# Kernel tuning notes

Measured on AMD Instinct MI355X. Metric: run time of the kernel, lower is better.

## Reference

```python
import jax, jax.numpy as jnp
import numpy as np

DIM = 1024
HEADS = 8
DIM_HEAD = 128
SCALE = DIM_HEAD ** -0.5
EPS = 1e-10
ROPE_THETA = 10000.0


def _rope_cos_sin(n, d, dtype):
    # lucidrains rotary-embedding-torch: interleaved freqs, repeated pairwise
    inv_freq = 1.0 / (ROPE_THETA ** (jnp.arange(0, d, 2, dtype=jnp.float32) / d))
    freqs = jnp.arange(n, dtype=jnp.float32)[:, None] * inv_freq[None, :]  # [n, d/2]
    freqs = jnp.repeat(freqs, 2, axis=-1)  # [n, d] interleaved (f0,f0,f1,f1,...)
    return jnp.cos(freqs).astype(dtype), jnp.sin(freqs).astype(dtype)


def _rotate_half(x):
    x = x.reshape(*x.shape[:-1], -1, 2)
    x1, x2 = x[..., 0], x[..., 1]
    return jnp.stack((-x2, x1), axis=-1).reshape(*x.shape[:-2], -1)


def _apply_rope(t, cos, sin):
    return t * cos + _rotate_half(t) * sin


def setup_inputs() -> dict:
    key = jax.random.key(0)
    k1, k2, k3, k4, k5 = jax.random.split(key, 5)
    b, n = 2, 2048
    return {
        "x": jax.random.normal(k1, (b, n, DIM), dtype=jnp.float32),
        "gamma": jnp.ones((DIM,), dtype=jnp.float32),
        "w_qkv": jax.random.normal(k2, (3 * HEADS * DIM_HEAD, DIM), dtype=jnp.float32) * 0.02,
        "w_out": jax.random.normal(k3, (DIM, HEADS * DIM_HEAD), dtype=jnp.float32) * 0.02,
        "head_gates": jnp.ones((HEADS,), dtype=jnp.float32) * 10.0,
        "mem_kv": jax.random.normal(k4, (b, HEADS, DIM_HEAD, DIM_HEAD), dtype=jnp.float32),
        "mem_norm": jax.random.uniform(k5, (b, HEADS, DIM_HEAD), dtype=jnp.float32) + 0.5,
    }


def _retrieve(t, mem_kv, mem_norm):
    # t: [b,h,n,dk] -> [b,h,n,dv]
    numer = jnp.einsum('bhnk,bhkv->bhnv', t, mem_kv)
    denom = jnp.einsum('bhnk,bhk->bhn', t, mem_norm)
    return numer / jnp.clip(denom, EPS, None)[..., None]


def reference(x, gamma, w_qkv, w_out, head_gates, mem_kv, mem_norm):
    b, n, _ = x.shape
    # RMSNorm (F.normalize * sqrt(dim) * gamma)
    xn = x / jnp.clip(jnp.linalg.norm(x, axis=-1, keepdims=True), 1e-12, None)
    xn = xn * (DIM ** 0.5) * gamma
    # qkv projection, split heads: 'b n (qkv h d) -> qkv b h n d'
    qkv = xn @ w_qkv.T  # [b,n,3*h*d]
    qkv = qkv.reshape(b, n, 3, HEADS, DIM_HEAD).transpose(2, 0, 3, 1, 4)
    q, k, v = qkv[0], qkv[1], qkv[2]

    cos, sin = _rope_cos_sin(n, DIM_HEAD, x.dtype)
    q_rot = _apply_rope(q * SCALE, cos, sin)
    k_rot = _apply_rope(k, cos, sin)

    sim = jnp.einsum('bhid,bhjd->bhij', q_rot, k_rot)
    causal = jnp.triu(jnp.ones((n, n), dtype=bool), 1)
    sim = jnp.where(causal, jnp.finfo(sim.dtype).min, sim)
    attn = jax.nn.softmax(sim, axis=-1)
    out = jnp.einsum('bhij,bhjd->bhid', attn, v)

    # linear-attention feature map on UNrotated, unscaled q/k
    qf = jax.nn.elu(q) + 1.0
    kf = jax.nn.elu(k) + 1.0

    # gated retrieval from past memories
    mem_out = _retrieve(qf, mem_kv, mem_norm)
    gates = jax.nn.sigmoid(head_gates)[None, :, None, None]
    out = out * gates + mem_out * (1.0 - gates)

    out = out.transpose(0, 2, 1, 3).reshape(b, n, HEADS * DIM_HEAD)
    out = out @ w_out.T

    # delta rule memory update
    delta_v = _retrieve(kf, mem_kv, mem_norm)
    v_new = v - delta_v
    new_kv = jnp.einsum('bhnk,bhnv->bhkv', kf, v_new) + mem_kv
    new_norm = kf.sum(axis=2) + mem_norm
    return out, new_kv, new_norm
```

## Files before the change

kernel.cpp:

```cpp
#include <hip/hip_runtime.h>
#include <hip/hip_bf16.h>

#define B_ 2
#define N_ 2048
#define H_ 8
#define DH_ 128
#define D_ 1024
#define NO_ 3072
#define SCALE_ 0.08838834764831845f

typedef __bf16 bf16;
typedef __bf16 bf16x4 __attribute__((ext_vector_type(4)));
typedef __bf16 bf16x8 __attribute__((ext_vector_type(8)));
typedef float f32x4 __attribute__((ext_vector_type(4)));

__device__ inline f32x4 mfma16(bf16x8 a, bf16x8 b, f32x4 c) {
  return __builtin_amdgcn_mfma_f32_16x16x32_bf16(a, b, c, 0, 0, 0);
}

__device__ inline float elu1(float x) { return x > 0.f ? x + 1.f : __expf(x); }

__device__ inline void gl_lds16(const bf16* g, bf16* l) {
  __builtin_amdgcn_global_load_lds(
      (const __attribute__((address_space(1))) unsigned int*)g,
      (__attribute__((address_space(3))) unsigned int*)l, 16, 0, 0);
}

__global__ __launch_bounds__(256) void k_rmsnorm(const float* __restrict__ x,
                                                 const float* __restrict__ gamma,
                                                 bf16* __restrict__ xn) {
  int row = blockIdx.x;
  int t = threadIdx.x;
  const float4* xr = (const float4*)(x + (size_t)row * D_);
  float4 xv = xr[t];
  float ss = xv.x*xv.x + xv.y*xv.y + xv.z*xv.z + xv.w*xv.w;
#pragma unroll
  for (int m = 1; m < 64; m <<= 1) ss += __shfl_xor(ss, m);
  __shared__ float sred[4];
  if ((t & 63) == 0) sred[t >> 6] = ss;
  __syncthreads();
  float tot = sred[0] + sred[1] + sred[2] + sred[3];
  float scale = 32.0f / fmaxf(sqrtf(tot), 1e-12f);
  float4 gv = ((const float4*)gamma)[t];
  bf16x4 ov;
  ov[0] = (bf16)(xv.x * scale * gv.x);
  ov[1] = (bf16)(xv.y * scale * gv.y);
  ov[2] = (bf16)(xv.z * scale * gv.z);
  ov[3] = (bf16)(xv.w * scale * gv.w);
  *(bf16x4*)(xn + (size_t)row * D_ + t * 4) = ov;
}

__global__ void k_cvtW(const float4* __restrict__ a, bf16x4* __restrict__ oa, int na4,
                       const float4* __restrict__ b, bf16x4* __restrict__ ob, int nb4) {
  int i = blockIdx.x * blockDim.x + threadIdx.x;
  if (i < na4) {
    float4 v = a[i];
    bf16x4 o;
    o[0] = (bf16)v.x; o[1] = (bf16)v.y; o[2] = (bf16)v.z; o[3] = (bf16)v.w;
    oa[i] = o;
  } else {
    int j = i - na4;
    if (j < nb4) {
      float4 v = b[j];
      bf16x4 o;
      o[0] = (bf16)v.x; o[1] = (bf16)v.y; o[2] = (bf16)v.z; o[3] = (bf16)v.w;
      ob[j] = o;
    }
  }
}

__global__ __launch_bounds__(256) void k_mkvT(const float* __restrict__ mem_kv,
                                              const float* __restrict__ mem_norm,
                                              bf16* __restrict__ mkvT,
                                              float* __restrict__ out_kv,
                                              float* __restrict__ out_norm) {
  int bh = blockIdx.x;
  int t = threadIdx.x;
  int v = t & 127, khalf = t >> 7;
  const float* src = mem_kv + (size_t)bh * DH_ * DH_;
  bf16* dst = mkvT + (size_t)bh * DH_ * DH_ + (size_t)v * DH_ + khalf * 64;
#pragma unroll
  for (int kk8 = 0; kk8 < 8; kk8++) {
    int k0 = khalf * 64 + kk8 * 8;
    bf16x8 o;
#pragma unroll
    for (int e = 0; e < 8; e++) o[e] = (bf16)src[(size_t)(k0 + e) * DH_ + v];
    *(bf16x8*)(dst + kk8 * 8) = o;
  }
  const float4* s4 = (const float4*)src;
  float4* d4 = (float4*)(out_kv + (size_t)bh * DH_ * DH_);
#pragma unroll
  for (int i = 0; i < 16; i++) d4[t + i * 256] = s4[t + i * 256];
  if (t < DH_) out_norm[(size_t)bh * DH_ + t] = mem_norm[(size_t)bh * DH_ + t];
}

template <typename OT>
__global__ __launch_bounds__(256) void k_gemm_lds(const bf16* __restrict__ A,
                                                  const bf16* __restrict__ B,
                                                  OT* __restrict__ C,
                                                  int M, int Nn, int K) {
  __shared__ __align__(16) bf16 sA[128 * 32];
  __shared__ __align__(16) bf16 sB[128 * 32];
  int t = threadIdx.x;
  int w = t >> 6, lane = t & 63, quad = lane >> 4, l16 = lane & 15;
  int lin = blockIdx.y * gridDim.x + blockIdx.x;
  int cpx = (gridDim.x * gridDim.y) >> 3;
  int swz = (lin & 7) * cpx + (lin >> 3);
  int bx = swz % gridDim.x, by = swz / gridDim.x;
  int m0 = by * 128, n0 = bx * 128;
  int wr = (w & 1) * 64, wc = (w >> 1) * 64;
  f32x4 zf = {0.f, 0.f, 0.f, 0.f};
  f32x4 acc[4][4];
#pragma unroll
  for (int a = 0; a < 4; a++)
#pragma unroll
    for (int c = 0; c < 4; c++) acc[a][c] = zf;
  int srow = w * 16 + (lane >> 2);
  int scol = (lane & 3) * 8;
  const bf16* gA = A + (size_t)(m0 + srow) * K + scol;
  const bf16* gB = B + (size_t)(n0 + srow) * K + scol;
  bf16* lA0 = sA + (size_t)w * 16 * 32;
  bf16* lA1 = sA + (size_t)(64 + w * 16) * 32;
  bf16* lB0 = sB + (size_t)w * 16 * 32;
  bf16* lB1 = sB + (size_t)(64 + w * 16) * 32;
  for (int k0 = 0; k0 < K; k0 += 32) {
    __syncthreads();
    gl_lds16(gA + k0, lA0);
    gl_lds16(gA + (size_t)64 * K + k0, lA1);
    gl_lds16(gB + k0, lB0);
    gl_lds16(gB + (size_t)64 * K + k0, lB1);
    __syncthreads();
    bf16x8 af[4], bfr[4];
#pragma unroll
    for (int mt = 0; mt < 4; mt++)
      af[mt] = *(const bf16x8*)(sA + (wr + mt * 16 + l16) * 32 + quad * 8);
#pragma unroll
    for (int nt = 0; nt < 4; nt++)
      bfr[nt] = *(const bf16x8*)(sB + (wc + nt * 16 + l16) * 32 + quad * 8);
#pragma unroll
    for (int mt = 0; mt < 4; mt++)
#pragma unroll
      for (int nt = 0; nt < 4; nt++)
        acc[mt][nt] = mfma16(af[mt], bfr[nt], acc[mt][nt]);
  }
#pragma unroll
  for (int mt = 0; mt < 4; mt++)
#pragma unroll
    for (int nt = 0; nt < 4; nt++) {
      int row = m0 + wr + mt * 16 + quad * 4;
      int col = n0 + wc + nt * 16 + l16;
      OT* cp = C + (size_t)row * Nn + col;
#pragma unroll
      for (int r = 0; r < 4; r++) cp[(size_t)r * Nn] = (OT)acc[mt][nt][r];
    }
}

__global__ __launch_bounds__(256) void k_prep2(const bf16* __restrict__ qkv,
                                               const float* __restrict__ mem_norm,
                                               bf16* __restrict__ qr, bf16* __restrict__ kr,
                                               bf16* __restrict__ vT, bf16* __restrict__ kfT,
                                               float* __restrict__ qden, float* __restrict__ kden) {
  __shared__ __align__(16) bf16 sQ[64 * 136], sK[64 * 136], sV[64 * 136];
  __shared__ float smn[128];
  int n0 = blockIdx.x * 64, h = blockIdx.y, b = blockIdx.z;
  size_t bh = (size_t)b * H_ + h;
  int t = threadIdx.x;
#pragma unroll
  for (int p = 0; p < 4; p++) {
    int i = p * 256 + t;
    int row = i >> 4, c16 = i & 15;
    size_t base = ((size_t)b * N_ + n0 + row) * NO_ + (size_t)h * DH_;
    ((uint4*)sQ)[row * 17 + c16] = *((const uint4*)(qkv + base) + c16);
    ((uint4*)sK)[row * 17 + c16] = *((const uint4*)(qkv + base + D_) + c16);
    ((uint4*)sV)[row * 17 + c16] = *((const uint4*)(qkv + base + 2 * D_) + c16);
  }
  if (t < 128) smn[t] = mem_norm[bh * DH_ + t];
  __syncthreads();
  int row = t >> 1, h2 = t & 1, d0 = h2 * 64;
  int n = n0 + row;
  float sq = 0.f, sk = 0.f;
  const float cexp = 13.287712379549449f / 128.0f;
#pragma unroll 2
  for (int c = 0; c < 8; c++) {
    bf16x8 q8 = *(const bf16x8*)(sQ + row * 136 + d0 + c * 8);
    bf16x8 k8 = *(const bf16x8*)(sK + row * 136 + d0 + c * 8);
    bf16x8 qo, ko, kf8;
#pragma unroll
    for (int e = 0; e < 8; e += 2) {
      int d = d0 + c * 8 + e;
      float invf = exp2f(-(float)d * cexp);
      float ang = (float)n * invf;
      float sn, cs;
      __sincosf(ang, &sn, &cs);
      float qx = (float)q8[e] * SCALE_, qy = (float)q8[e + 1] * SCALE_;
      qo[e]     = (bf16)(qx * cs - qy * sn);
      qo[e + 1] = (bf16)(qy * cs + qx * sn);
      float kx = (float)k8[e], ky = (float)k8[e + 1];
      ko[e]     = (bf16)(kx * cs - ky * sn);
      ko[e + 1] = (bf16)(ky * cs + kx * sn);
      float f0 = elu1(kx), f1 = elu1(ky);
      kf8[e] = (bf16)f0; kf8[e + 1] = (bf16)f1;
      sk += f0 * smn[d] + f1 * smn[d + 1];
      sq += elu1((float)q8[e]) * smn[d] + elu1((float)q8[e + 1]) * smn[d + 1];
    }
    *(bf16x8*)(qr + (bh * N_ + n) * DH_ + d0 + c * 8) = qo;
    *(bf16x8*)(kr + (bh * N_ + n) * DH_ + d0 + c * 8) = ko;
    *(bf16x8*)(sK + row * 136 + d0 + c * 8) = kf8;
  }
  sq += __shfl_xor(sq, 1);
  sk += __shfl_xor(sk, 1);
  if (h2 == 0) { qden[bh * N_ + n] = sq; kden[bh * N_ + n] = sk; }
  __syncthreads();
  int d = t >> 1, part = t & 1;
#pragma unroll
  for (int v8 = 0; v8 < 4; v8++) {
    bf16x8 okf, ov;
#pragma unroll
    for (int e = 0; e < 8; e++) {
      int nn = part * 32 + v8 * 8 + e;
      okf[e] = sK[nn * 136 + d];
      ov[e]  = sV[nn * 136 + d];
    }
    size_t o = (bh * DH_ + d) * N_ + n0 + part * 32 + v8 * 8;
    *(bf16x8*)(kfT + o) = okf;
    *(bf16x8*)(vT + o)  = ov;
  }
}

__global__ __launch_bounds__(256) void k_attn2(const bf16* __restrict__ qr,
                                               const bf16* __restrict__ kr,
                                               const bf16* __restrict__ vT,
                                               bf16* __restrict__ attn_out,
                                               bf16* __restrict__ pO,
                                               float* __restrict__ pstat) {
  __shared__ __align__(16) bf16 sK[64 * 128];
  __shared__ __align__(16) bf16 sV[128 * 64];
  int L = blockIdx.x;
  int x = (L & 7) * 160 + (L >> 3);
  size_t bh = x / 80;
  int e = x % 80;
  int qt, c;
  if (e < 32)      { qt = 31 - (e >> 2); c = e & 3; }
  else if (e < 56) { int u = e - 32; qt = 23 - u / 3; c = u % 3; }
  else if (e < 72) { int u = e - 56; qt = 15 - (u >> 1); c = u & 1; }
  else             { qt = 7 - (e - 72); c = 0; }
  int jt0 = c * 8;
  int jt1 = min(jt0 + 8, qt + 1);

  int t = threadIdx.x;
  int w = t >> 6, lane = t & 63, quad = lane >> 4, l16 = lane & 15;
  int qlo = qt * 64 + w * 16;

  bf16x8 qfrag[4];
  const bf16* qrow = qr + (bh * N_ + qlo + l16) * DH_;
#pragma unroll
  for (int s = 0; s < 4; s++) qfrag[s] = *(const bf16x8*)(qrow + s * 32 + quad * 8);

  f32x4 zf = {0.f, 0.f, 0.f, 0.f};
  f32x4 o[8];
#pragma unroll
  for (int i = 0; i < 8; i++) o[i] = zf;
  float mrow = -1e30f, lrow = 0.f;

  int krow = lane >> 4, kc16 = lane & 15;
  int vrow = lane >> 3, vc8 = lane & 7;

  for (int jt = jt0; jt < jt1; jt++) {
    __syncthreads();
#pragma unroll
    for (int j = 0; j < 4; j++) {
      int prow = w * 16 + j * 4 + krow;
      int grow = (prow & 32) | ((prow & 12) << 1) | ((prow & 16) >> 2) | (prow & 3);
      const bf16* src = kr + (bh * N_ + (size_t)jt * 64 + grow) * DH_ + (kc16 ^ (prow & 7)) * 8;
      gl_lds16(src, sK + (w * 16 + j * 4) * 128);
    }
#pragma unroll
    for (int j = 0; j < 4; j++) {
      int row = w * 32 + j * 8 + vrow;
      const bf16* src = vT + (bh * DH_ + row) * N_ + (size_t)jt * 64 + (vc8 ^ (row & 7)) * 8;
      gl_lds16(src, sV + (w * 32 + j * 8) * 64);
    }
    __syncthreads();

    f32x4 sf[4];
#pragma unroll
    for (int nt = 0; nt < 4; nt++) sf[nt] = zf;
    __builtin_amdgcn_s_setprio(1);
#pragma unroll
    for (int s = 0; s < 4; s++) {
#pragma unroll
      for (int nt = 0; nt < 4; nt++) {
        int row = nt * 16 + l16;
        bf16x8 kf = *(const bf16x8*)(sK + row * 128 + ((s * 32 + quad * 8) ^ ((row & 7) << 3)));
        sf[nt] = mfma16(kf, qfrag[s], sf[nt]);
      }
    }
    __builtin_amdgcn_s_setprio(0);
    if (jt == qt) {
      int qg = qlo + l16;
#pragma unroll
      for (int nt = 0; nt < 4; nt++) {
        int kb = jt * 64 + ((nt >> 1) << 5) + (quad << 3) + ((nt & 1) << 2);
#pragma unroll
        for (int r = 0; r < 4; r++) {
          if (kb + r > qg) sf[nt][r] = -1e30f;
        }
      }
    }
    float tm = -1e30f;
#pragma unroll
    for (int nt = 0; nt < 4; nt++)
#pragma unroll
      for (int r = 0; r < 4; r++) tm = fmaxf(tm, sf[nt][r]);
    tm = fmaxf(tm, __shfl_xor(tm, 16));
    tm = fmaxf(tm, __shfl_xor(tm, 32));
    float mn = fmaxf(mrow, tm);
    float alpha = __expf(mrow - mn);
    float rs = 0.f;
#pragma unroll
    for (int nt = 0; nt < 4; nt++)
#pragma unroll
      for (int r = 0; r < 4; r++) {
        float p = __expf(sf[nt][r] - mn);
        sf[nt][r] = p;
        rs += p;
      }
    rs += __shfl_xor(rs, 16);
    rs += __shfl_xor(rs, 32);
    lrow = lrow * alpha + rs;
    mrow = mn;
#pragma unroll
    for (int i = 0; i < 8; i++) {
      o[i][0] *= alpha; o[i][1] *= alpha;
      o[i][2] *= alpha; o[i][3] *= alpha;
    }
    bf16x8 pa0, pa1;
#pragma unroll
    for (int r = 0; r < 4; r++) {
      pa0[r]     = (bf16)sf[0][r];
      pa0[4 + r] = (bf16)sf[1][r];
      pa1[r]     = (bf16)sf[2][r];
      pa1[4 + r] = (bf16)sf[3][r];
    }
    __builtin_amdgcn_s_setprio(1);
#pragma unroll
    for (int vt = 0; vt < 8; vt++) {
      int row0 = vt * 16 + l16;
      bf16x8 b0 = *(const bf16x8*)(sV + row0 * 64 + ((quad * 8) ^ ((row0 & 7) << 3)));
      bf16x8 b1 = *(const bf16x8*)(sV + row0 * 64 + ((32 + quad * 8) ^ ((row0 & 7) << 3)));
      o[vt] = mfma16(b0, pa0, o[vt]);
      o[vt] = mfma16(b1, pa1, o[vt]);
    }
    __builtin_amdgcn_s_setprio(0);
  }

  if (qt < 8) {
    float inv = 1.f / lrow;
    int qg = qlo + l16;
#pragma unroll
    for (int vt = 0; vt < 8; vt++) {
      bf16x4 ov;
#pragma unroll
      for (int r = 0; r < 4; r++) ov[r] = (bf16)(o[vt][r] * inv);
      *(bf16x4*)(attn_out + (bh * N_ + qg) * DH_ + vt * 16 + quad * 4) = ov;
    }
  } else {
    int cid = ((int)bh * 24 + qt - 8) * 4 + c;
    int lr = w * 16 + l16;
    if (quad == 0) {
      float2 st = {mrow, lrow};
      *(float2*)(pstat + ((size_t)cid * 64 + lr) * 2) = st;
    }
#pragma unroll
    for (int vt = 0; vt < 8; vt++) {
      bf16x4 ov;
#pragma unroll
      for (int r = 0; r < 4; r++) ov[r] = (bf16)o[vt][r];
      *(bf16x4*)(pO + ((size_t)cid * 64 + lr) * DH_ + vt * 16 + quad * 4) = ov;
    }
  }
}

__global__ __launch_bounds__(256) void k_combine(const bf16* __restrict__ pO,
                                                 const float* __restrict__ pstat,
                                                 bf16* __restrict__ attn_out) {
  int x = blockIdx.x;
  int bh = x / 24, qi = x % 24;
  int qt = 8 + qi;
  int nch = (qt + 8) / 8;
  int t = threadIdx.x;
  int row = t >> 2, dseg = (t & 3) * 32;
  int cidb = (bh * 24 + qi) * 4;
  float ms[4], ls[4];
  float mg = -1e30f;
#pragma unroll 4
  for (int c = 0; c < nch; c++) {
    float2 st = *(const float2*)(pstat + ((size_t)(cidb + c) * 64 + row) * 2);
    ms[c] = st.x; ls[c] = st.y;
    mg = fmaxf(mg, st.x);
  }
  float L = 0.f, wc[4];
#pragma unroll 4
  for (int c = 0; c < nch; c++) { wc[c] = __expf(ms[c] - mg); L += ls[c] * wc[c]; }
  float inv = 1.f / L;
  float acc[32];
#pragma unroll
  for (int i = 0; i < 32; i++) acc[i] = 0.f;
#pragma unroll 4
  for (int c = 0; c < nch; c++) {
    const bf16x8* p = (const bf16x8*)(pO + ((size_t)(cidb + c) * 64 + row) * DH_ + dseg);
#pragma unroll
    for (int j = 0; j < 4; j++) {
      bf16x8 v = p[j];
#pragma unroll
      for (int e2 = 0; e2 < 8; e2++) acc[j * 8 + e2] += wc[c] * (float)v[e2];
    }
  }
  bf16* dst = attn_out + ((size_t)bh * N_ + qt * 64 + row) * DH_ + dseg;
#pragma unroll
  for (int j = 0; j < 4; j++) {
    bf16x8 ov;
#pragma unroll
    for (int e2 = 0; e2 < 8; e2++) ov[e2] = (bf16)(acc[j * 8 + e2] * inv);
    *(bf16x8*)(dst + j * 8) = ov;
  }
}

#define SMT_STRIDE 136
#define VNSTR 138
__global__ __launch_bounds__(256) void k_retrieve2(const bf16* __restrict__ qkv,
                                                   const bf16* __restrict__ mkvT,
                                                   const float* __restrict__ qden,
                                                   const float* __restrict__ kden,
                                                   const bf16* __restrict__ attn,
                                                   const float* __restrict__ hg,
                                                   bf16* __restrict__ comb,
                                                   bf16* __restrict__ vnT) {
  __shared__ __align__(16) bf16 smT[DH_ * SMT_STRIDE];
  __shared__ bf16 sVn[64 * VNSTR];
  int h = blockIdx.y, b = blockIdx.z;
  size_t bh = (size_t)b * H_ + h;
  int t = threadIdx.x;
  int w = t >> 6, lane = t & 63, quad = lane >> 4, l16 = lane & 15;
  int n0 = blockIdx.x * 64;

  {
    const uint4* src = (const uint4*)(mkvT + bh * DH_ * DH_);
    uint4* dst = (uint4*)smT;
#pragma unroll
    for (int it = 0; it < 8; it++) {
      int i = t + it * 256;
      int row = i >> 4, col = i & 15;
      dst[row * 17 + col] = src[i];
    }
  }

  int nrow = n0 + w * 16 + l16;
  const bf16* base = qkv + ((size_t)b * N_ + nrow) * NO_ + h * DH_;
  bf16x8 qa[4], ka[4];
#pragma unroll
  for (int s = 0; s < 4; s++) {
    int k0 = s * 32 + quad * 8;
    bf16x8 q8 = *(const bf16x8*)(base + k0);
    bf16x8 k8 = *(const bf16x8*)(base + D_ + k0);
    bf16x8 qo, ko;
#pragma unroll
    for (int e2 = 0; e2 < 8; e2++) {
      qo[e2] = (bf16)elu1((float)q8[e2]);
      ko[e2] = (bf16)elu1((float)k8[e2]);
    }
    qa[s] = qo; ka[s] = ko;
  }

  __syncthreads();
  f32x4 zf = {0.f, 0.f, 0.f, 0.f};
  f32x4 accq[8], acck[8];
#pragma unroll
  for (int vt = 0; vt < 8; vt++) { accq[vt] = zf; acck[vt] = zf; }
#pragma unroll
  for (int vt = 0; vt < 8; vt++) {
#pragma unroll
    for (int s = 0; s < 4; s++) {
      bf16x8 bfr = *(const bf16x8*)(smT + (vt * 16 + l16) * SMT_STRIDE + s * 32 + quad * 8);
      accq[vt] = mfma16(qa[s], bfr, accq[vt]);
      acck[vt] = mfma16(ka[s], bfr, acck[vt]);
    }
  }

  float g = 1.f / (1.f + __expf(-hg[h]));
#pragma unroll
  for (int r = 0; r < 4; r++) {
    int nl = w * 16 + quad * 4 + r;
    int n = n0 + nl;
    size_t m = (size_t)b * N_ + n;
    float qd = fmaxf(qden[bh * N_ + n], 1e-10f);
    float kd = fmaxf(kden[bh * N_ + n], 1e-10f);
#pragma unroll
    for (int vt = 0; vt < 8; vt++) {
      int v = vt * 16 + l16;
      float mo = accq[vt][r] / qd;
      float ov = (float)attn[(bh * N_ + n) * DH_ + v];
      comb[m * D_ + h * DH_ + v] = (bf16)(ov * g + mo * (1.f - g));
      float vv = (float)qkv[m * NO_ + 2 * D_ + h * DH_ + v];
      sVn[nl * VNSTR + v] = (bf16)(vv - acck[vt][r] / kd);
    }
  }
  __syncthreads();
  int d = t >> 1, part = t & 1;
#pragma unroll
  for (int v8 = 0; v8 < 4; v8++) {
    bf16x8 ov;
#pragma unroll
    for (int e2 = 0; e2 < 8; e2++) ov[e2] = sVn[(part * 32 + v8 * 8 + e2) * VNSTR + d];
    *(bf16x8*)(vnT + (bh * DH_ + d) * N_ + n0 + part * 32 + v8 * 8) = ov;
  }
}

#define GSTR 40
__global__ __launch_bounds__(256) void k_newkv2(const bf16* __restrict__ kfT,
                                                const bf16* __restrict__ vnT,
                                                float* __restrict__ out_kv,
                                                float* __restrict__ out_norm) {
  __shared__ __align__(16) bf16 sA[128 * GSTR];
  __shared__ __align__(16) bf16 sB[128 * GSTR];
  int t = threadIdx.x;
  int w = t >> 6, lane = t & 63, quad = lane >> 4, l16 = lane & 15;
  size_t bh = (size_t)blockIdx.z * H_ + blockIdx.y;
  const bf16* A  = kfT + bh * DH_ * N_;
  const bf16* Bm = vnT + bh * DH_ * N_;
  int wr = (w & 1) * 64, wc = (w >> 1) * 64;
  f32x4 zf = {0.f, 0.f, 0.f, 0.f};
  f32x4 acc[4][4];
#pragma unroll
  for (int a = 0; a < 4; a++)
#pragma unroll
    for (int c = 0; c < 4; c++) acc[a][c] = zf;
  int trow = t >> 2, tc = t & 3;
  float sn0 = 0.f, sn1 = 0.f;
  int kend = (blockIdx.x + 1) * 128;
  for (int k0 = blockIdx.x * 128; k0 < kend; k0 += 32) {
    __syncthreads();
    uint4 va0 = *((const uint4*)(A + (size_t)trow * N_ + k0) + tc);
    uint4 va1 = *((const uint4*)(A + (size_t)(trow + 64) * N_ + k0) + tc);
    ((uint4*)sA)[trow * 5 + tc]        = va0;
    ((uint4*)sA)[(trow + 64) * 5 + tc] = va1;
    ((uint4*)sB)[trow * 5 + tc]        = *((const uint4*)(Bm + (size_t)trow * N_ + k0) + tc);
    ((uint4*)sB)[(trow + 64) * 5 + tc] = *((const uint4*)(Bm + (size_t)(trow + 64) * N_ + k0) + tc);
    bf16x8 x0 = *(bf16x8*)&va0, x1 = *(bf16x8*)&va1;
#pragma unroll
    for (int e = 0; e < 8; e++) { sn0 += (float)x0[e]; sn1 += (float)x1[e]; }
    __syncthreads();
    bf16x8 af[4], bfr[4];
#pragma unroll
    for (int mt = 0; mt < 4; mt++)
      af[mt] = *(const bf16x8*)(sA + (wr + mt * 16 + l16) * GSTR + quad * 8);
#pragma unroll
    for (int nt = 0; nt < 4; nt++)
      bfr[nt] = *(const bf16x8*)(sB + (wc + nt * 16 + l16) * GSTR + quad * 8);
#pragma unroll
    for (int mt = 0; mt < 4; mt++)
#pragma unroll
      for (int nt = 0; nt < 4; nt++)
        acc[mt][nt] = mfma16(af[mt], bfr[nt], acc[mt][nt]);
  }
  sn0 += __shfl_xor(sn0, 1); sn0 += __shfl_xor(sn0, 2);
  sn1 += __shfl_xor(sn1, 1); sn1 += __shfl_xor(sn1, 2);
  if (tc == 0) {
    atomicAdd(out_norm + bh * DH_ + trow, sn0);
    atomicAdd(out_norm + bh * DH_ + trow + 64, sn1);
  }
  float* obh = out_kv + bh * DH_ * DH_;
#pragma unroll
  for (int mt = 0; mt < 4; mt++)
#pragma unroll
    for (int nt = 0; nt < 4; nt++) {
      int row = wr + mt * 16 + quad * 4;
      int col = wc + nt * 16 + l16;
#pragma unroll
      for (int r = 0; r < 4; r++)
        atomicAdd(obh + (size_t)(row + r) * DH_ + col, acc[mt][nt][r]);
    }
}

extern "C" void kernel_launch(void* const* d_in, const int* in_sizes, int n_in,
                              void* d_out, int out_size, void* d_ws, size_t ws_size,
                              hipStream_t stream) {
  const float* x        = (const float*)d_in[0];
  const float* gamma    = (const float*)d_in[1];
  const float* w_qkv    = (const float*)d_in[2];
  const float* w_out    = (const float*)d_in[3];
  const float* hg       = (const float*)d_in[4];
  const float* mem_kv   = (const float*)d_in[5];
  const float* mem_norm = (const float*)d_in[6];
  float* out      = (float*)d_out;
  float* out_kv   = out + (size_t)B_ * N_ * D_;
  float* out_norm = out_kv + (size_t)B_ * H_ * DH_ * DH_;

  char* ws = (char*)d_ws;
  size_t off = 0;
  auto alloc = [&](size_t bytes) -> void* {
    void* p = ws + off;
    off += (bytes + 255) & ~(size_t)255;
    return p;
  };
  bf16*  xn   = (bf16*)alloc((size_t)B_ * N_ * D_ * 2);
  bf16*  wqb  = (bf16*)alloc((size_t)NO_ * D_ * 2);
  bf16*  wob  = (bf16*)alloc((size_t)D_ * D_ * 2);
  bf16*  qkvb = (bf16*)alloc((size_t)B_ * N_ * NO_ * 2);
  bf16*  qr   = (bf16*)alloc((size_t)B_ * H_ * N_ * DH_ * 2);
  bf16*  kr   = (bf16*)alloc((size_t)B_ * H_ * N_ * DH_ * 2);
  bf16*  vT   = (bf16*)alloc((size_t)B_ * H_ * DH_ * N_ * 2);
  bf16*  kfT  = (bf16*)alloc((size_t)B_ * H_ * DH_ * N_ * 2);
  float* qden = (float*)alloc((size_t)B_ * H_ * N_ * 4);
  float* kden = (float*)alloc((size_t)B_ * H_ * N_ * 4);
  bf16*  attnb= (bf16*)alloc((size_t)B_ * H_ * N_ * DH_ * 2);
  bf16*  mkvT = (bf16*)alloc((size_t)B_ * H_ * DH_ * DH_ * 2);
  size_t pO_bytes    = (size_t)1536 * 64 * DH_ * 2;
  size_t pstat_bytes = (size_t)1536 * 64 * 2 * 4;
  size_t comb_bytes  = (size_t)B_ * N_ * D_ * 2;
  size_t vnT_bytes   = (size_t)B_ * H_ * DH_ * N_ * 2;
  size_t union_bytes = pO_bytes + pstat_bytes;
  if (comb_bytes + vnT_bytes > union_bytes) union_bytes = comb_bytes + vnT_bytes;
  char* uni = (char*)alloc(union_bytes);
  bf16*  pO    = (bf16*)uni;
  float* pstat = (float*)(uni + pO_bytes);
  bf16*  comb  = (bf16*)uni;
  bf16*  vnT   = (bf16*)(uni + comb_bytes);
  (void)in_sizes; (void)n_in; (void)out_size; (void)ws_size;

  k_rmsnorm<<<dim3(B_ * N_), 256, 0, stream>>>(x, gamma, xn);
  k_cvtW<<<(NO_ * D_ / 4 + D_ * D_ / 4 + 255) / 256, 256, 0, stream>>>(
      (const float4*)w_qkv, (bf16x4*)wqb, NO_ * D_ / 4,
      (const float4*)w_out, (bf16x4*)wob, D_ * D_ / 4);
  k_mkvT<<<dim3(B_ * H_), 256, 0, stream>>>(mem_kv, mem_norm, mkvT, out_kv, out_norm);
  k_gemm_lds<bf16><<<dim3(NO_ / 128, B_ * N_ / 128), 256, 0, stream>>>(xn, wqb, qkvb, B_ * N_, NO_, D_);
  k_prep2<<<dim3(N_ / 64, H_, B_), 256, 0, stream>>>(qkvb, mem_norm, qr, kr, vT, kfT, qden, kden);
  k_attn2<<<dim3(1280), 256, 0, stream>>>(qr, kr, vT, attnb, pO, pstat);
  k_combine<<<dim3(384), 256, 0, stream>>>(pO, pstat, attnb);
  k_retrieve2<<<dim3(N_ / 64, H_, B_), 256, 0, stream>>>(qkvb, mkvT, qden, kden, attnb, hg, comb, vnT);
  k_gemm_lds<float><<<dim3(D_ / 128, B_ * N_ / 128), 256, 0, stream>>>(comb, wob, out, B_ * N_, D_, D_);
  k_newkv2<<<dim3(16, H_, B_), 256, 0, stream>>>(kfT, vnT, out_kv, out_norm);
}
```

Measured before the change: 267.9 us.

## Fuse split-attention combine into retrieve and deepen GEMM K-tile with swizzled LDS

Removes the separate k_combine launch by merging the partial softmax chunks (pO/pstat) directly inside k_retrieve2 for the later query tiles. The bf16 GEMM now loads a 64-wide K slice per iteration with an XOR-swizzled LDS layout, halving the number of barrier pairs and reducing LDS bank conflicts. Workspace aliasing changes so comb and vnT reuse the xn and kr buffers, which are dead by that point. The GEMM doubles its LDS use, which may lower occupancy. The retrieve kernel also gets more uncoalesced pO reads.

```diff
diff --git a/kernel.cpp b/kernel.cpp
--- a/kernel.cpp
+++ b/kernel.cpp
@@ -99,8 +99,8 @@
                                                   const bf16* __restrict__ B,
                                                   OT* __restrict__ C,
                                                   int M, int Nn, int K) {
-  __shared__ __align__(16) bf16 sA[128 * 32];
-  __shared__ __align__(16) bf16 sB[128 * 32];
+  __shared__ __align__(16) bf16 sA[128 * 64];
+  __shared__ __align__(16) bf16 sB[128 * 64];
   int t = threadIdx.x;
   int w = t >> 6, lane = t & 63, quad = lane >> 4, l16 = lane & 15;
   int lin = blockIdx.y * gridDim.x + blockIdx.x;
@@ -115,33 +115,36 @@
   for (int a = 0; a < 4; a++)
 #pragma unroll
     for (int c = 0; c < 4; c++) acc[a][c] = zf;
-  int srow = w * 16 + (lane >> 2);
-  int scol = (lane & 3) * 8;
-  const bf16* gA = A + (size_t)(m0 + srow) * K + scol;
-  const bf16* gB = B + (size_t)(n0 + srow) * K + scol;
-  bf16* lA0 = sA + (size_t)w * 16 * 32;
-  bf16* lA1 = sA + (size_t)(64 + w * 16) * 32;
-  bf16* lB0 = sB + (size_t)w * 16 * 32;
-  bf16* lB1 = sB + (size_t)(64 + w * 16) * 32;
-  for (int k0 = 0; k0 < K; k0 += 32) {
+  int r8 = lane >> 3, c8 = lane & 7;
+  for (int k0 = 0; k0 < K; k0 += 64) {
     __syncthreads();
-    gl_lds16(gA + k0, lA0);
-    gl_lds16(gA + (size_t)64 * K + k0, lA1);
-    gl_lds16(gB + k0, lB0);
-    gl_lds16(gB + (size_t)64 * K + k0, lB1);
+#pragma unroll
+    for (int j = 0; j < 4; j++) {
+      int prow = w * 32 + j * 8 + r8;
+      int co = (c8 ^ (prow & 7)) * 8;
+      gl_lds16(A + (size_t)(m0 + prow) * K + k0 + co, sA + (w * 32 + j * 8) * 64);
+      gl_lds16(B + (size_t)(n0 + prow) * K + k0 + co, sB + (w * 32 + j * 8) * 64);
+    }
     __syncthreads();
-    bf16x8 af[4], bfr[4];
-#pragma unroll
-    for (int mt = 0; mt < 4; mt++)
-      af[mt] = *(const bf16x8*)(sA + (wr + mt * 16 + l16) * 32 + quad * 8);
-#pragma unroll
-    for (int nt = 0; nt < 4; nt++)
-      bfr[nt] = *(const bf16x8*)(sB + (wc + nt * 16 + l16) * 32 + quad * 8);
-#pragma unroll
-    for (int mt = 0; mt < 4; mt++)
-#pragma unroll
-      for (int nt = 0; nt < 4; nt++)
-        acc[mt][nt] = mfma16(af[mt], bfr[nt], acc[mt][nt]);
+#pragma unroll
+    for (int ks = 0; ks < 2; ks++) {
+      bf16x8 af[4], bfr[4];
+#pragma unroll
+      for (int mt = 0; mt < 4; mt++) {
+        int row = wr + mt * 16 + l16;
+        af[mt] = *(const bf16x8*)(sA + row * 64 + ((ks * 32 + quad * 8) ^ ((row & 7) << 3)));
+      }
+#pragma unroll
+      for (int nt = 0; nt < 4; nt++) {
+        int row = wc + nt * 16 + l16;
+        bfr[nt] = *(const bf16x8*)(sB + row * 64 + ((ks * 32 + quad * 8) ^ ((row & 7) << 3)));
+      }
+#pragma unroll
+      for (int mt = 0; mt < 4; mt++)
+#pragma unroll
+        for (int nt = 0; nt < 4; nt++)
+          acc[mt][nt] = mfma16(af[mt], bfr[nt], acc[mt][nt]);
+    }
   }
 #pragma unroll
   for (int mt = 0; mt < 4; mt++)
@@ -381,51 +384,6 @@
   }
 }
 
-__global__ __launch_bounds__(256) void k_combine(const bf16* __restrict__ pO,
-                                                 const float* __restrict__ pstat,
-                                                 bf16* __restrict__ attn_out) {
-  int x = blockIdx.x;
-  int bh = x / 24, qi = x % 24;
-  int qt = 8 + qi;
-  int nch = (qt + 8) / 8;
-  int t = threadIdx.x;
-  int row = t >> 2, dseg = (t & 3) * 32;
-  int cidb = (bh * 24 + qi) * 4;
-  float ms[4], ls[4];
-  float mg = -1e30f;
-#pragma unroll 4
-  for (int c = 0; c < nch; c++) {
-    float2 st = *(const float2*)(pstat + ((size_t)(cidb + c) * 64 + row) * 2);
-    ms[c] = st.x; ls[c] = st.y;
-    mg = fmaxf(mg, st.x);
-  }
-  float L = 0.f, wc[4];
-#pragma unroll 4
-  for (int c = 0; c < nch; c++) { wc[c] = __expf(ms[c] - mg); L += ls[c] * wc[c]; }
-  float inv = 1.f / L;
-  float acc[32];
-#pragma unroll
-  for (int i = 0; i < 32; i++) acc[i] = 0.f;
-#pragma unroll 4
-  for (int c = 0; c < nch; c++) {
-    const bf16x8* p = (const bf16x8*)(pO + ((size_t)(cidb + c) * 64 + row) * DH_ + dseg);
-#pragma unroll
-    for (int j = 0; j < 4; j++) {
-      bf16x8 v = p[j];
-#pragma unroll
-      for (int e2 = 0; e2 < 8; e2++) acc[j * 8 + e2] += wc[c] * (float)v[e2];
-    }
-  }
-  bf16* dst = attn_out + ((size_t)bh * N_ + qt * 64 + row) * DH_ + dseg;
-#pragma unroll
-  for (int j = 0; j < 4; j++) {
-    bf16x8 ov;
-#pragma unroll
-    for (int e2 = 0; e2 < 8; e2++) ov[e2] = (bf16)(acc[j * 8 + e2] * inv);
-    *(bf16x8*)(dst + j * 8) = ov;
-  }
-}
-
 #define SMT_STRIDE 136
 #define VNSTR 138
 __global__ __launch_bounds__(256) void k_retrieve2(const bf16* __restrict__ qkv,
@@ -433,6 +391,8 @@
                                                    const float* __restrict__ qden,
                                                    const float* __restrict__ kden,
                                                    const bf16* __restrict__ attn,
+                                                   const bf16* __restrict__ pO,
+                                                   const float* __restrict__ pstat,
                                                    const float* __restrict__ hg,
                                                    bf16* __restrict__ comb,
                                                    bf16* __restrict__ vnT) {
@@ -442,7 +402,11 @@
   size_t bh = (size_t)b * H_ + h;
   int t = threadIdx.x;
   int w = t >> 6, lane = t & 63, quad = lane >> 4, l16 = lane & 15;
-  int n0 = blockIdx.x * 64;
+  int qt = blockIdx.x;
+  int n0 = qt * 64;
+  bool direct = (qt < 8);
+  int cidb = ((int)bh * 24 + qt - 8) * 4;
+  int nch = (qt + 8) / 8;
 
   {
     const uint4* src = (const uint4*)(mkvT + bh * DH_ * DH_);
@@ -495,11 +459,35 @@
     size_t m = (size_t)b * N_ + n;
     float qd = fmaxf(qden[bh * N_ + n], 1e-10f);
     float kd = fmaxf(kden[bh * N_ + n], 1e-10f);
+    float wcs[4] = {0.f, 0.f, 0.f, 0.f};
+    float cinv = 1.f;
+    if (!direct) {
+      float ms[4], ls[4], mg = -1e30f;
+#pragma unroll 4
+      for (int cc = 0; cc < nch; cc++) {
+        float2 st = *(const float2*)(pstat + ((size_t)(cidb + cc) * 64 + nl) * 2);
+        ms[cc] = st.x; ls[cc] = st.y;
+        mg = fmaxf(mg, st.x);
+      }
+      float Lg = 0.f;
+#pragma unroll 4
+      for (int cc = 0; cc < nch; cc++) { wcs[cc] = __expf(ms[cc] - mg); Lg += ls[cc] * wcs[cc]; }
+      cinv = 1.f / Lg;
+    }
 #pragma unroll
     for (int vt = 0; vt < 8; vt++) {
       int v = vt * 16 + l16;
       float mo = accq[vt][r] / qd;
-      float ov = (float)attn[(bh * N_ + n) * DH_ + v];
+      float ov;
+      if (direct) {
+        ov = (float)attn[(bh * N_ + n) * DH_ + v];
+      } else {
+        float s = 0.f;
+#pragma unroll 4
+        for (int cc = 0; cc < nch; cc++)
+          s += wcs[cc] * (float)pO[((size_t)(cidb + cc) * 64 + nl) * DH_ + v];
+        ov = s * cinv;
+      }
       comb[m * D_ + h * DH_ + v] = (bf16)(ov * g + mo * (1.f - g));
       float vv = (float)qkv[m * NO_ + 2 * D_ + h * DH_ + v];
       sVn[nl * VNSTR + v] = (bf16)(vv - acck[vt][r] / kd);
@@ -615,17 +603,10 @@
   float* kden = (float*)alloc((size_t)B_ * H_ * N_ * 4);
   bf16*  attnb= (bf16*)alloc((size_t)B_ * H_ * N_ * DH_ * 2);
   bf16*  mkvT = (bf16*)alloc((size_t)B_ * H_ * DH_ * DH_ * 2);
-  size_t pO_bytes    = (size_t)1536 * 64 * DH_ * 2;
-  size_t pstat_bytes = (size_t)1536 * 64 * 2 * 4;
-  size_t comb_bytes  = (size_t)B_ * N_ * D_ * 2;
-  size_t vnT_bytes   = (size_t)B_ * H_ * DH_ * N_ * 2;
-  size_t union_bytes = pO_bytes + pstat_bytes;
-  if (comb_bytes + vnT_bytes > union_bytes) union_bytes = comb_bytes + vnT_bytes;
-  char* uni = (char*)alloc(union_bytes);
-  bf16*  pO    = (bf16*)uni;
-  float* pstat = (float*)(uni + pO_bytes);
-  bf16*  comb  = (bf16*)uni;
-  bf16*  vnT   = (bf16*)(uni + comb_bytes);
+  bf16*  pO    = (bf16*)alloc((size_t)1536 * 64 * DH_ * 2);
+  float* pstat = (float*)alloc((size_t)1536 * 64 * 2 * 4);
+  bf16*  comb = xn;
+  bf16*  vnT  = kr;
   (void)in_sizes; (void)n_in; (void)out_size; (void)ws_size;
 
   k_rmsnorm<<<dim3(B_ * N_), 256, 0, stream>>>(x, gamma, xn);
@@ -636,8 +617,7 @@
   k_gemm_lds<bf16><<<dim3(NO_ / 128, B_ * N_ / 128), 256, 0, stream>>>(xn, wqb, qkvb, B_ * N_, NO_, D_);
   k_prep2<<<dim3(N_ / 64, H_, B_), 256, 0, stream>>>(qkvb, mem_norm, qr, kr, vT, kfT, qden, kden);
   k_attn2<<<dim3(1280), 256, 0, stream>>>(qr, kr, vT, attnb, pO, pstat);
-  k_combine<<<dim3(384), 256, 0, stream>>>(pO, pstat, attnb);
-  k_retrieve2<<<dim3(N_ / 64, H_, B_), 256, 0, stream>>>(qkvb, mkvT, qden, kden, attnb, hg, comb, vnT);
+  k_retrieve2<<<dim3(N_ / 64, H_, B_), 256, 0, stream>>>(qkvb, mkvT, qden, kden, attnb, pO, pstat, hg, comb, vnT);
   k_gemm_lds<float><<<dim3(D_ / 128, B_ * N_ / 128), 256, 0, stream>>>(comb, wob, out, B_ * N_, D_, D_);
   k_newkv2<<<dim3(16, H_, B_), 256, 0, stream>>>(kfT, vnT, out_kv, out_norm);
 }
```

Measured after the change: 276.4 us. 1.03x slower.
